# Kernel tuning notes

Hardware: AMD Instinct MI355X
Metric: run time of the kernel (lower is better)

Reference implementation:

```python
import jax, jax.numpy as jnp
import numpy as np

B, N = 16, 262144          # batch, pixels per image (512*512)
N_CLASSES = 150            # ADE20K-like
N_PRED = 4096              # global predicted segment ids


def setup_inputs() -> dict:
    key = jax.random.key(0)
    k1, k2 = jax.random.split(key)
    predseg = jax.random.randint(k1, (B, N), 0, N_PRED, dtype=jnp.int64)
    targetseg = jax.random.randint(k2, (B, N), 0, N_CLASSES, dtype=jnp.int64)
    # eye buffer from the module (self._targets), treated as a float param
    targets = jnp.eye(N_CLASSES, dtype=jnp.float32)
    return {
        "predseg": predseg,
        "targetseg": targetseg,
        "targets": targets,
        "n_classes": N_CLASSES,
        "n_pred_ids": N_PRED,
    }


def reference(predseg, targetseg, targets, n_classes, n_pred_ids):
    b, n = predseg.shape
    T = b * n_classes  # number of distinct target segment ids (b_idx*maxseg + class)
    pred = predseg.reshape(-1)
    # target id = batch_index * n_classes + class label, exactly as in torch
    tgt = (jnp.arange(b, dtype=predseg.dtype)[:, None] * n_classes + targetseg).reshape(-1)

    # Dense co-occurrence histogram O[p, t] = #pixels with pred==p and target==t.
    # Equivalent to the sort/unique pipeline: pairs with O==0 had IoU contribution 0.
    flat = pred * T + tgt
    O = jnp.zeros((n_pred_ids * T,), jnp.float32).at[flat].add(1.0)
    O = O.reshape(n_pred_ids, T)

    n_pred = O.sum(axis=1, keepdims=True)    # pixels per pred segment
    n_tgt = O.sum(axis=0, keepdims=True)     # pixels per target segment
    iou = jnp.where(O > 0, O / (n_pred + n_tgt - O), 0.0)  # [P, B*C]

    # scatter_reduce of iou * targets[class] over pred ids ==
    # sum over batch then matmul with the class-target matrix
    iou_pc = iou.reshape(n_pred_ids, b, n_classes).sum(axis=1)  # [P, C]
    out = iou_pc @ targets                                      # [P, C]
    den = out.sum(axis=-1, keepdims=True)
    return out / den
```

## Files before the change

kernel.cpp:

```cpp
#include <hip/hip_runtime.h>

#define B_    16
#define N_    262144
#define NC    150
#define NP    4096
#define T_    (B_ * NC)
#define TOTAL (B_ * N_)

#define PBKT   256
#define SEGS   1024
#define SEGPIX 4096
#define QT     9600

typedef unsigned int u32;
typedef unsigned short u16;

__global__ __launch_bounds__(256) void partition_kernel(const int* __restrict__ pred,
                                                        const int* __restrict__ tgt,
                                                        u16* __restrict__ recSeg,
                                                        u32* __restrict__ metaArr,
                                                        u16* __restrict__ ntPart) {
    __shared__ u32 keybuf[SEGPIX];
    __shared__ u16 rankbuf[SEGPIX];
    __shared__ u16 staging[SEGPIX];
    __shared__ u32 cnt[PBKT];
    __shared__ u32 lstart[PBKT];
    __shared__ u32 nth[NC];
    __shared__ u32 wsum[4];

    int tid = threadIdx.x;
    int blk = blockIdx.x;
    cnt[tid] = 0;
    if (tid < NC) nth[tid] = 0;
    __syncthreads();

    int base = blk * SEGPIX;
    int b_img = base >> 18;
    const int4* pred4 = (const int4*)pred;
    const int4* tgt4  = (const int4*)tgt;

    #pragma unroll
    for (int k = 0; k < 4; ++k) {
        int vi = (base >> 2) + k * 256 + tid;
        int4 pv = pred4[vi];
        int4 tv = tgt4[vi];
        int pe[4] = {pv.x, pv.y, pv.z, pv.w};
        int te[4] = {tv.x, tv.y, tv.z, tv.w};
        #pragma unroll
        for (int e = 0; e < 4; ++e) {
            int p = pe[e];
            u32 bkt = (u32)(p >> 4);
            u32 lk  = (u32)((p & 15) * T_ + b_img * NC + te[e]);
            int flat = (k * 256 + tid) * 4 + e;
            u32 rank = atomicAdd(&cnt[bkt], 1u);
            keybuf[flat]  = (bkt << 16) | lk;
            rankbuf[flat] = (u16)rank;
            atomicAdd(&nth[te[e]], 1u);
        }
    }
    __syncthreads();

    {
        u32 myc = cnt[tid];
        u32 v = myc;
        #pragma unroll
        for (int o = 1; o < 64; o <<= 1) {
            u32 t = __shfl_up(v, o);
            if ((tid & 63) >= o) v += t;
        }
        if ((tid & 63) == 63) wsum[tid >> 6] = v;
        __syncthreads();
        u32 woff = 0;
        #pragma unroll
        for (int w = 0; w < 3; ++w) woff += (w < (tid >> 6)) ? wsum[w] : 0;
        u32 ex = v + woff - myc;
        lstart[tid] = ex;
        metaArr[blk * PBKT + tid] = (ex << 16) | myc;
    }
    if (tid < NC) ntPart[blk * 160 + tid] = (u16)nth[tid];
    __syncthreads();

    #pragma unroll
    for (int k = 0; k < 16; ++k) {
        int flat = tid * 16 + k;
        u32 v = keybuf[flat];
        staging[lstart[v >> 16] + (u32)rankbuf[flat]] = (u16)(v & 0xFFFFu);
    }
    __syncthreads();

    {
        const uint4* s4 = (const uint4*)staging;
        uint4* d4 = (uint4*)(recSeg + (size_t)blk * SEGPIX);
        d4[tid]       = s4[tid];
        d4[tid + 256] = s4[tid + 256];
    }
}

__global__ __launch_bounds__(256) void ntreduce(const u16* __restrict__ ntPart,
                                                u32* __restrict__ gNT) {
    int img = blockIdx.x;
    int c = threadIdx.x;
    if (c < NC) {
        u32 s = 0;
        #pragma unroll 8
        for (int b2 = 0; b2 < SEGS / B_; ++b2)
            s += ntPart[(img * (SEGS / B_) + b2) * 160 + c];
        gNT[img * NC + c] = s;
    }
}

__global__ __launch_bounds__(256, 7) void iou_kernel(const u16* __restrict__ recSeg,
                                                     const u32* __restrict__ metaArr,
                                                     const u32* __restrict__ gNT,
                                                     const float* __restrict__ targets,
                                                     float* __restrict__ out) {
    __shared__ u32 hist[QT / 2];
    __shared__ float npred_s[4];
    __shared__ float iou_pc[4][NC];
    __shared__ float4 wred[4];

    int tid = threadIdx.x;
    int bkt = blockIdx.x & 255;
    int q   = blockIdx.x >> 8;
    u32 lo = (u32)(q * QT);

    {
        uint4 z4 = make_uint4(0u, 0u, 0u, 0u);
        uint4* h4 = (uint4*)hist;
        for (int j = tid; j < QT / 8; j += 256) h4[j] = z4;
    }
    __syncthreads();

    for (int s = tid; s < SEGS; s += 256) {
        u32 m  = metaArr[s * PBKT + bkt];
        u32 ls = m >> 16;
        u32 n  = m & 0xFFFFu;
        if (!n) continue;
        u32 je = ls + n;
        const u16* segp = recSeg + (size_t)s * SEGPIX;
        for (u32 j = ls & ~7u; j < je; j += 8) {
            uint4 v = *(const uint4*)(segp + j);
            u32 words[4] = {v.x, v.y, v.z, v.w};
            #pragma unroll
            for (int w = 0; w < 4; ++w) {
                #pragma unroll
                for (int h = 0; h < 2; ++h) {
                    u32 idx = j + (u32)(w * 2 + h);
                    if (idx >= ls && idx < je) {
                        u32 lk = ((words[w] >> (h * 16)) & 0xFFFFu) - lo;
                        if (lk < (u32)QT)
                            atomicAdd(&hist[lk >> 1], (lk & 1u) ? 65536u : 1u);
                    }
                }
            }
        }
    }
    __syncthreads();

    {
        int pl = tid >> 6, lane = tid & 63;
        u32 s = 0;
        for (int w = lane; w < T_ / 2; w += 64) {
            u32 v = hist[pl * (T_ / 2) + w];
            s += (v & 0xFFFFu) + (v >> 16);
        }
        #pragma unroll
        for (int o = 32; o > 0; o >>= 1) s += __shfl_xor(s, o);
        if (lane == 0) npred_s[pl] = (float)s;
    }
    __syncthreads();

    for (int idx = tid; idx < 4 * NC; idx += 256) {
        int pl = idx / NC, cls = idx - pl * NC;
        float np = npred_s[pl];
        float acc = 0.f;
        #pragma unroll
        for (int b = 0; b < B_; ++b) {
            int lk = pl * T_ + b * NC + cls;
            u32 w = hist[lk >> 1];
            u32 v = (lk & 1) ? (w >> 16) : (w & 0xFFFFu);
            if (v) {
                float fv = (float)v;
                acc += fv * __builtin_amdgcn_rcpf(np + (float)gNT[b * NC + cls] - fv);
            }
        }
        iou_pc[pl][cls] = acc;
    }
    __syncthreads();

    float o0 = 0.f, o1 = 0.f, o2 = 0.f, o3 = 0.f;
    if (tid < NC) {
        for (int k = 0; k < NC; ++k) {
            float tv = targets[k * NC + tid];
            o0 += iou_pc[0][k] * tv;
            o1 += iou_pc[1][k] * tv;
            o2 += iou_pc[2][k] * tv;
            o3 += iou_pc[3][k] * tv;
        }
    }

    {
        float4 v = (tid < NC) ? make_float4(o0, o1, o2, o3)
                              : make_float4(0.f, 0.f, 0.f, 0.f);
        #pragma unroll
        for (int o = 32; o > 0; o >>= 1) {
            v.x += __shfl_xor(v.x, o);
            v.y += __shfl_xor(v.y, o);
            v.z += __shfl_xor(v.z, o);
            v.w += __shfl_xor(v.w, o);
        }
        if ((tid & 63) == 0) wred[tid >> 6] = v;
    }
    __syncthreads();
    float4 den;
    {
        float4 a = wred[0], b = wred[1], c = wred[2], d = wred[3];
        den = make_float4(a.x + b.x + c.x + d.x, a.y + b.y + c.y + d.y,
                          a.z + b.z + c.z + d.z, a.w + b.w + c.w + d.w);
    }

    if (tid < NC) {
        size_t ob = (size_t)(bkt * 16 + q * 4) * NC + tid;
        out[ob + 0 * NC] = o0 * __builtin_amdgcn_rcpf(den.x);
        out[ob + 1 * NC] = o1 * __builtin_amdgcn_rcpf(den.y);
        out[ob + 2 * NC] = o2 * __builtin_amdgcn_rcpf(den.z);
        out[ob + 3 * NC] = o3 * __builtin_amdgcn_rcpf(den.w);
    }
}

extern "C" void kernel_launch(void* const* d_in, const int* in_sizes, int n_in,
                              void* d_out, int out_size, void* d_ws, size_t ws_size,
                              hipStream_t stream) {
    const int*   pred    = (const int*)d_in[0];
    const int*   tgt     = (const int*)d_in[1];
    const float* targets = (const float*)d_in[2];
    float*       out     = (float*)d_out;

    u16* recSeg  = (u16*)d_ws;
    u32* metaArr = (u32*)(recSeg + (size_t)SEGS * SEGPIX);
    u16* ntPart  = (u16*)(metaArr + SEGS * PBKT);
    u32* gNT     = (u32*)(ntPart + SEGS * 160);

    partition_kernel<<<SEGS, 256, 0, stream>>>(pred, tgt, recSeg, metaArr, ntPart);
    ntreduce<<<B_, 256, 0, stream>>>(ntPart, gNT);
    iou_kernel<<<PBKT * 4, 256, 0, stream>>>(recSeg, metaArr, gNT, targets, out);
}
```

Baseline: 54.80 us.

## Partition pixels into finer sub-buckets so IoU blocks read only their quarter

The partition kernel now buckets pixels by pred>>2 into 1024 sub-buckets, with two 16-bit counters packed per shared word, and writes per-sub-bucket metadata. Before, each IoU block scanned every record of a 16-id bucket and kept only a quarter. Now each block reads just the records for its 4 pred ids, cutting recSeg traffic and the wasted range checks in the IoU kernel. In exchange the metadata array grows fourfold, and each IoU block issues more but smaller segment reads.

New measurement: 54.59 us. No clear change (-0.4%).

```diff
diff --git a/kernel.cpp b/kernel.cpp
--- a/kernel.cpp
+++ b/kernel.cpp
@@ -7,7 +7,7 @@
 #define T_    (B_ * NC)
 #define TOTAL (B_ * N_)
 
-#define PBKT   256
+#define NSUB   1024
 #define SEGS   1024
 #define SEGPIX 4096
 #define QT     9600
@@ -23,14 +23,15 @@
     __shared__ u32 keybuf[SEGPIX];
     __shared__ u16 rankbuf[SEGPIX];
     __shared__ u16 staging[SEGPIX];
-    __shared__ u32 cnt[PBKT];
-    __shared__ u32 lstart[PBKT];
+    __shared__ u32 cnt32[NSUB / 2];
+    __shared__ u32 lstart[NSUB];
     __shared__ u32 nth[NC];
     __shared__ u32 wsum[4];
 
     int tid = threadIdx.x;
     int blk = blockIdx.x;
-    cnt[tid] = 0;
+    cnt32[tid] = 0;
+    cnt32[tid + 256] = 0;
     if (tid < NC) nth[tid] = 0;
     __syncthreads();
 
@@ -49,20 +50,23 @@
         #pragma unroll
         for (int e = 0; e < 4; ++e) {
             int p = pe[e];
-            u32 bkt = (u32)(p >> 4);
+            u32 sub = (u32)(p >> 2);
             u32 lk  = (u32)((p & 15) * T_ + b_img * NC + te[e]);
             int flat = (k * 256 + tid) * 4 + e;
-            u32 rank = atomicAdd(&cnt[bkt], 1u);
-            keybuf[flat]  = (bkt << 16) | lk;
-            rankbuf[flat] = (u16)rank;
+            u32 shift = (sub & 1u) * 16u;
+            u32 old = atomicAdd(&cnt32[sub >> 1], 1u << shift);
+            keybuf[flat]  = (sub << 16) | lk;
+            rankbuf[flat] = (u16)((old >> shift) & 0xFFFFu);
             atomicAdd(&nth[te[e]], 1u);
         }
     }
     __syncthreads();
 
     {
-        u32 myc = cnt[tid];
-        u32 v = myc;
+        u32 w0 = cnt32[2 * tid], w1 = cnt32[2 * tid + 1];
+        u32 c0 = w0 & 0xFFFFu, c1 = w0 >> 16, c2 = w1 & 0xFFFFu, c3 = w1 >> 16;
+        u32 tot = c0 + c1 + c2 + c3;
+        u32 v = tot;
         #pragma unroll
         for (int o = 1; o < 64; o <<= 1) {
             u32 t = __shfl_up(v, o);
@@ -73,9 +77,13 @@
         u32 woff = 0;
         #pragma unroll
         for (int w = 0; w < 3; ++w) woff += (w < (tid >> 6)) ? wsum[w] : 0;
-        u32 ex = v + woff - myc;
-        lstart[tid] = ex;
-        metaArr[blk * PBKT + tid] = (ex << 16) | myc;
+        u32 run = v + woff - tot;
+        uint4 mv;
+        lstart[4 * tid + 0] = run; mv.x = (run << 16) | c0; run += c0;
+        lstart[4 * tid + 1] = run; mv.y = (run << 16) | c1; run += c1;
+        lstart[4 * tid + 2] = run; mv.z = (run << 16) | c2; run += c2;
+        lstart[4 * tid + 3] = run; mv.w = (run << 16) | c3;
+        ((uint4*)metaArr)[blk * 256 + tid] = mv;
     }
     if (tid < NC) ntPart[blk * 160 + tid] = (u16)nth[tid];
     __syncthreads();
@@ -120,9 +128,8 @@
     __shared__ float4 wred[4];
 
     int tid = threadIdx.x;
-    int bkt = blockIdx.x & 255;
-    int q   = blockIdx.x >> 8;
-    u32 lo = (u32)(q * QT);
+    int sub = blockIdx.x;
+    u32 lo = (u32)((sub & 3) * QT);
 
     {
         uint4 z4 = make_uint4(0u, 0u, 0u, 0u);
@@ -132,7 +139,7 @@
     __syncthreads();
 
     for (int s = tid; s < SEGS; s += 256) {
-        u32 m  = metaArr[s * PBKT + bkt];
+        u32 m  = metaArr[s * NSUB + sub];
         u32 ls = m >> 16;
         u32 n  = m & 0xFFFFu;
         if (!n) continue;
@@ -220,7 +227,7 @@
     }
 
     if (tid < NC) {
-        size_t ob = (size_t)(bkt * 16 + q * 4) * NC + tid;
+        size_t ob = (size_t)((sub >> 2) * 16 + (sub & 3) * 4) * NC + tid;
         out[ob + 0 * NC] = o0 * __builtin_amdgcn_rcpf(den.x);
         out[ob + 1 * NC] = o1 * __builtin_amdgcn_rcpf(den.y);
         out[ob + 2 * NC] = o2 * __builtin_amdgcn_rcpf(den.z);
@@ -238,10 +245,10 @@
 
     u16* recSeg  = (u16*)d_ws;
     u32* metaArr = (u32*)(recSeg + (size_t)SEGS * SEGPIX);
-    u16* ntPart  = (u16*)(metaArr + SEGS * PBKT);
+    u16* ntPart  = (u16*)(metaArr + (size_t)SEGS * NSUB);
     u32* gNT     = (u32*)(ntPart + SEGS * 160);
 
     partition_kernel<<<SEGS, 256, 0, stream>>>(pred, tgt, recSeg, metaArr, ntPart);
     ntreduce<<<B_, 256, 0, stream>>>(ntPart, gNT);
-    iou_kernel<<<PBKT * 4, 256, 0, stream>>>(recSeg, metaArr, gNT, targets, out);
-}
+    iou_kernel<<<NSUB, 256, 0, stream>>>(recSeg, metaArr, gNT, targets, out);
+}
```
